# Optimization experiments

Hardware: AMD Instinct MI355X
Metric: run time of the kernel (lower is better)

Reference implementation:

```python
import jax, jax.numpy as jnp
import numpy as np

NUM_CLASSES = 19
TEMPERATURE = 0.2


def setup_inputs() -> dict:
    key = jax.random.key(0)
    k1, k2, k3 = jax.random.split(key, 3)
    fea = jax.random.normal(k1, (8, 256, 128, 128), dtype=jnp.float32)
    res = jax.random.normal(k2, (8, 19, 128, 128), dtype=jnp.float32)
    q = jax.random.normal(k3, (NUM_CLASSES, 256, 2975), dtype=jnp.float32)
    # buffers are L2-normalized along the feature (inner_planes) dim at init
    queues = q / jnp.maximum(jnp.linalg.norm(q, axis=1, keepdims=True), 1e-12)
    return {"fea": fea, "res": res, "queues": queues}


def _contrast_loss(fea, res, queues):
    # fea: [bs, C, H, W], res: [bs, K, H, W] logits, queues: [K, C, Q]
    bs, C = fea.shape[0], fea.shape[1]
    pred = jnp.argmax(res, axis=1).reshape(bs, -1)          # [bs, HW]
    ff = fea.reshape(bs, C, -1)                              # [bs, C, HW]

    # masked per-class region pooling across the whole batch (pred == val)
    onehot = (pred[:, :, None] == jnp.arange(NUM_CLASSES)[None, None, :]).astype(fea.dtype)  # [bs, HW, K]
    counts = onehot.sum(axis=(0, 1))                         # [K]
    sums = jnp.einsum('bcp,bpk->kc', ff, onehot)             # [K, C]
    keys = sums / jnp.maximum(counts, 1.0)[:, None]          # masked mean per class
    # F.normalize(keys, dim=1) with eps=1e-12
    keys = keys / jnp.maximum(jnp.linalg.norm(keys, axis=1, keepdims=True), 1e-12)

    # l_pos = q[:,None] * queue_c ; l_neg = q[:,None] * sum_{c'!=c} queue_c'
    qsum = queues.sum(axis=0)                                # [C, Q]
    l_pos = keys[:, :, None] * queues                        # [K, C, Q]
    l_neg = keys[:, :, None] * (qsum[None] - queues)         # [K, C, Q]
    logits = jnp.concatenate([l_pos, l_neg], axis=2) / TEMPERATURE  # [K, C, 2Q]

    # CrossEntropyLoss with labels all zero: mean over rows of (logsumexp - logit_0)
    lse = jax.nn.logsumexp(logits, axis=2)                   # [K, C]
    per_class = jnp.mean(lse - logits[:, :, 0], axis=1)      # [K]

    # original sums loss only over classes present in pred
    present = counts > 0
    return jnp.sum(jnp.where(present, per_class, jnp.zeros_like(per_class)))


def reference(fea, res, queues):
    contrast_loss = _contrast_loss(fea, res, queues)
    return (res, contrast_loss)
```

## Files before the change

kernel.cpp:

```cpp
#include <hip/hip_runtime.h>

#define HW 16384
#define BS 8
#define NC 256
#define K  19
#define Q  2975
#define INV_T 5.0f
#define NCHUNK 4
#define QC 744
#define NB1 512

__global__ void __launch_bounds__(256) k1_argmax(const float* __restrict__ res,
                                                 float* __restrict__ out,
                                                 unsigned char* __restrict__ pred,
                                                 int* __restrict__ histb,
                                                 float* __restrict__ sums) {
    __shared__ int hist[K];
    int t = threadIdx.x;
    if (t < K) hist[t] = 0;
    __syncthreads();
    int gp = blockIdx.x * 256 + t;
    int b  = gp >> 14;
    int p  = gp & (HW - 1);
    const float* rb = res + (size_t)b * K * HW + p;
    float*       ob = out + (size_t)b * K * HW + p;
    float best = rb[0];
    int   bk   = 0;
    ob[0] = best;
    #pragma unroll
    for (int k = 1; k < K; ++k) {
        float v = rb[(size_t)k * HW];
        ob[(size_t)k * HW] = v;
        if (v > best) { best = v; bk = k; }
    }
    pred[gp] = (unsigned char)bk;
    atomicAdd(&hist[bk], 1);
    if (blockIdx.x == 0) {
        for (int i = t; i < K * NC; i += 256) sums[i] = 0.f;
    }
    __syncthreads();
    if (t < K) histb[t * NB1 + blockIdx.x] = hist[t];
}

__global__ void __launch_bounds__(256) k2_pool(const float* __restrict__ fea,
                                               const unsigned char* __restrict__ pred,
                                               float* __restrict__ sums) {
    __shared__ float acc[K * 256];
    int t = threadIdx.x;
    int b = blockIdx.x >> 8;
    int c = blockIdx.x & 255;
    #pragma unroll
    for (int k = 0; k < K; ++k) acc[k * 256 + t] = 0.f;
    __syncthreads();
    const float4* f4 = (const float4*)(fea + (size_t)(b * NC + c) * HW);
    const uchar4* p4 = (const uchar4*)(pred + (size_t)b * HW);
    for (int i = t; i < HW / 4; i += 256) {
        float4 v  = f4[i];
        uchar4 kk = p4[i];
        acc[kk.x * 256 + t] += v.x;
        acc[kk.y * 256 + t] += v.y;
        acc[kk.z * 256 + t] += v.z;
        acc[kk.w * 256 + t] += v.w;
    }
    __syncthreads();
    for (int s = 128; s > 0; s >>= 1) {
        for (int idx = t; idx < K * s; idx += 256) {
            int k = idx / s, j = idx - k * s;
            acc[k * 256 + j] += acc[k * 256 + j + s];
        }
        __syncthreads();
    }
    if (t < K) atomicAdd(&sums[t * 256 + c], acc[t * 256]);
}

__global__ void k3_keys(const float* __restrict__ sums, const int* __restrict__ histb,
                        float* __restrict__ keys_t, float* __restrict__ countsf) {
    int t = threadIdx.x, lane = t & 63, w = t >> 6;
    const float4* s4 = (const float4*)sums;
    float4*       o4 = (float4*)keys_t;
    for (int k = w; k < K; k += 4) {
        float cf = 0.f;
        #pragma unroll
        for (int j = 0; j < NB1 / 64; ++j)
            cf += (float)histb[k * NB1 + j * 64 + lane];
        float4 v = s4[k * 64 + lane];
        float ss = v.x * v.x + v.y * v.y + v.z * v.z + v.w * v.w;
        #pragma unroll
        for (int off = 32; off > 0; off >>= 1) {
            ss += __shfl_xor(ss, off, 64);
            cf += __shfl_xor(cf, off, 64);
        }
        float denom = fmaxf(sqrtf(ss), fmaxf(cf, 1.0f) * 1e-12f);
        float sc = INV_T / denom;
        v.x *= sc; v.y *= sc; v.z *= sc; v.w *= sc;
        o4[k * 64 + lane] = v;
        if (lane == 0) countsf[k] = cf;
    }
}

__global__ void __launch_bounds__(256, 4) k4_lse(const float* __restrict__ queues,
                                                 const float* __restrict__ keys_t,
                                                 float* __restrict__ spart,
                                                 float* __restrict__ pos0) {
    int t = threadIdx.x;
    int c = blockIdx.x;
    int chunk = blockIdx.y;
    int lane = t & 63, wv = t >> 6;

    float key[K], s[K];
    #pragma unroll
    for (int k = 0; k < K; ++k) {
        key[k] = keys_t[k * NC + c];
        s[k] = 0.f;
    }
    if (chunk == 0 && t < K)
        pos0[t * NC + c] = keys_t[t * NC + c] * queues[(size_t)(t * NC + c) * Q];

    int q0 = chunk * QC;
    int qhi = min(Q, q0 + QC);
    for (int q = q0 + t; q < qhi; q += 256) {
        float qv[K];
        float qs = 0.f;
        #pragma unroll
        for (int k = 0; k < K; ++k) {
            qv[k] = queues[(size_t)(k * NC + c) * Q + q];
            qs += qv[k];
        }
        #pragma unroll
        for (int k = 0; k < K; ++k) {
            float a  = key[k] * qv[k];
            float bn = fmaf(key[k], qs, -a);
            s[k] += __expf(a) + __expf(bn);
        }
    }

    __shared__ float sw[K][4];
    #pragma unroll
    for (int k = 0; k < K; ++k) {
        float sk = s[k];
        #pragma unroll
        for (int off = 32; off > 0; off >>= 1) sk += __shfl_xor(sk, off, 64);
        if (lane == 0) sw[k][wv] = sk;
    }
    __syncthreads();
    if (t < K)
        spart[((size_t)t * NC + c) * NCHUNK + chunk] = sw[t][0] + sw[t][1] + sw[t][2] + sw[t][3];
}

__global__ void k5_final(const float* __restrict__ spart, const float* __restrict__ pos0,
                         const float* __restrict__ countsf, float* __restrict__ loss) {
    int t = threadIdx.x;
    float acc = 0.f;
    #pragma unroll
    for (int k = 0; k < K; ++k) {
        float4 sp = ((const float4*)spart)[k * NC + t];
        float lse = logf(sp.x + sp.y + sp.z + sp.w);
        if (countsf[k] > 0.5f) acc += lse - pos0[k * NC + t];
    }
    __shared__ float red[256];
    red[t] = acc;
    __syncthreads();
    for (int s = 128; s > 0; s >>= 1) {
        if (t < s) red[t] += red[t + s];
        __syncthreads();
    }
    if (t == 0) *loss = red[0] * (1.0f / 256.0f);
}

extern "C" void kernel_launch(void* const* d_in, const int* in_sizes, int n_in,
                              void* d_out, int out_size, void* d_ws, size_t ws_size,
                              hipStream_t stream) {
    const float* fea    = (const float*)d_in[0];
    const float* res    = (const float*)d_in[1];
    const float* queues = (const float*)d_in[2];

    float* out  = (float*)d_out;
    float* loss = out + (size_t)BS * K * HW;

    char* ws = (char*)d_ws;
    float*         sums   = (float*)(ws);
    int*           histb  = (int*)(ws + 19456);
    float*         countsf= (float*)(ws + 58368);
    unsigned char* pred   = (unsigned char*)(ws + 58496);
    float*         keys_t = (float*)(ws + 189568);
    float*         spart  = (float*)(ws + 209024);
    float*         pos0   = (float*)(ws + 286848);

    hipLaunchKernelGGL(k1_argmax, dim3(NB1),        dim3(256), 0, stream, res, out, pred, histb, sums);
    hipLaunchKernelGGL(k2_pool,   dim3(BS * NC),    dim3(256), 0, stream, fea, pred, sums);
    hipLaunchKernelGGL(k3_keys,   dim3(1),          dim3(256), 0, stream, sums, histb, keys_t, countsf);
    hipLaunchKernelGGL(k4_lse,    dim3(NC, NCHUNK), dim3(256), 0, stream, queues, keys_t, spart, pos0);
    hipLaunchKernelGGL(k5_final,  dim3(1),          dim3(256), 0, stream, spart, pos0, countsf, loss);
}
```

Before: 62.15 us.

## Fold key normalization into lse kernel and simplify pooling reduction

Removes the single-block keys kernel by having each lse block recompute per-class norms from the pooled sums into shared memory, and moves class-count summation into the final kernel. The pooling kernel's multi-step shared-memory tree reduction is replaced by a strided add plus wave shuffle with per-wave atomics. This drops a kernel launch and many block barriers, at the cost of redundant norm computation in every lse block.

```diff
diff --git a/kernel.cpp b/kernel.cpp
--- a/kernel.cpp
+++ b/kernel.cpp
@@ -46,7 +46,7 @@
                                                const unsigned char* __restrict__ pred,
                                                float* __restrict__ sums) {
     __shared__ float acc[K * 256];
-    int t = threadIdx.x;
+    int t = threadIdx.x, lane = t & 63, w = t >> 6;
     int b = blockIdx.x >> 8;
     int c = blockIdx.x & 255;
     #pragma unroll
@@ -63,43 +63,17 @@
         acc[kk.w * 256 + t] += v.w;
     }
     __syncthreads();
-    for (int s = 128; s > 0; s >>= 1) {
-        for (int idx = t; idx < K * s; idx += 256) {
-            int k = idx / s, j = idx - k * s;
-            acc[k * 256 + j] += acc[k * 256 + j + s];
-        }
-        __syncthreads();
-    }
-    if (t < K) atomicAdd(&sums[t * 256 + c], acc[t * 256]);
-}
-
-__global__ void k3_keys(const float* __restrict__ sums, const int* __restrict__ histb,
-                        float* __restrict__ keys_t, float* __restrict__ countsf) {
-    int t = threadIdx.x, lane = t & 63, w = t >> 6;
-    const float4* s4 = (const float4*)sums;
-    float4*       o4 = (float4*)keys_t;
     for (int k = w; k < K; k += 4) {
-        float cf = 0.f;
+        float v = acc[k * 256 + lane]       + acc[k * 256 + lane + 64]
+                + acc[k * 256 + lane + 128] + acc[k * 256 + lane + 192];
         #pragma unroll
-        for (int j = 0; j < NB1 / 64; ++j)
-            cf += (float)histb[k * NB1 + j * 64 + lane];
-        float4 v = s4[k * 64 + lane];
-        float ss = v.x * v.x + v.y * v.y + v.z * v.z + v.w * v.w;
-        #pragma unroll
-        for (int off = 32; off > 0; off >>= 1) {
-            ss += __shfl_xor(ss, off, 64);
-            cf += __shfl_xor(cf, off, 64);
-        }
-        float denom = fmaxf(sqrtf(ss), fmaxf(cf, 1.0f) * 1e-12f);
-        float sc = INV_T / denom;
-        v.x *= sc; v.y *= sc; v.z *= sc; v.w *= sc;
-        o4[k * 64 + lane] = v;
-        if (lane == 0) countsf[k] = cf;
+        for (int off = 32; off > 0; off >>= 1) v += __shfl_xor(v, off, 64);
+        if (lane == 0) atomicAdd(&sums[k * NC + c], v);
     }
 }
 
 __global__ void __launch_bounds__(256, 4) k4_lse(const float* __restrict__ queues,
-                                                 const float* __restrict__ keys_t,
+                                                 const float* __restrict__ sums,
                                                  float* __restrict__ spart,
                                                  float* __restrict__ pos0) {
     int t = threadIdx.x;
@@ -107,14 +81,28 @@
     int chunk = blockIdx.y;
     int lane = t & 63, wv = t >> 6;
 
+    __shared__ float sc_sh[K];
+    for (int k = wv; k < K; k += 4) {
+        float ss = 0.f;
+        #pragma unroll
+        for (int j = 0; j < 4; ++j) {
+            float v = sums[k * NC + j * 64 + lane];
+            ss += v * v;
+        }
+        #pragma unroll
+        for (int off = 32; off > 0; off >>= 1) ss += __shfl_xor(ss, off, 64);
+        if (lane == 0) sc_sh[k] = INV_T / fmaxf(sqrtf(ss), 1e-12f);
+    }
+    __syncthreads();
+
     float key[K], s[K];
     #pragma unroll
     for (int k = 0; k < K; ++k) {
-        key[k] = keys_t[k * NC + c];
+        key[k] = sums[k * NC + c] * sc_sh[k];
         s[k] = 0.f;
     }
     if (chunk == 0 && t < K)
-        pos0[t * NC + c] = keys_t[t * NC + c] * queues[(size_t)(t * NC + c) * Q];
+        pos0[t * NC + c] = sums[t * NC + c] * sc_sh[t] * queues[(size_t)(t * NC + c) * Q];
 
     int q0 = chunk * QC;
     int qhi = min(Q, q0 + QC);
@@ -148,14 +136,25 @@
 }
 
 __global__ void k5_final(const float* __restrict__ spart, const float* __restrict__ pos0,
-                         const float* __restrict__ countsf, float* __restrict__ loss) {
-    int t = threadIdx.x;
+                         const int* __restrict__ histb, float* __restrict__ loss) {
+    __shared__ float cnt_sh[K];
+    int t = threadIdx.x, lane = t & 63, w = t >> 6;
+    for (int k = w; k < K; k += 4) {
+        float cf = 0.f;
+        #pragma unroll
+        for (int j = 0; j < NB1 / 64; ++j)
+            cf += (float)histb[k * NB1 + j * 64 + lane];
+        #pragma unroll
+        for (int off = 32; off > 0; off >>= 1) cf += __shfl_xor(cf, off, 64);
+        if (lane == 0) cnt_sh[k] = cf;
+    }
+    __syncthreads();
     float acc = 0.f;
     #pragma unroll
     for (int k = 0; k < K; ++k) {
         float4 sp = ((const float4*)spart)[k * NC + t];
         float lse = logf(sp.x + sp.y + sp.z + sp.w);
-        if (countsf[k] > 0.5f) acc += lse - pos0[k * NC + t];
+        if (cnt_sh[k] > 0.5f) acc += lse - pos0[k * NC + t];
     }
     __shared__ float red[256];
     red[t] = acc;
@@ -180,15 +179,12 @@
     char* ws = (char*)d_ws;
     float*         sums   = (float*)(ws);
     int*           histb  = (int*)(ws + 19456);
-    float*         countsf= (float*)(ws + 58368);
-    unsigned char* pred   = (unsigned char*)(ws + 58496);
-    float*         keys_t = (float*)(ws + 189568);
-    float*         spart  = (float*)(ws + 209024);
-    float*         pos0   = (float*)(ws + 286848);
+    unsigned char* pred   = (unsigned char*)(ws + 58368);
+    float*         spart  = (float*)(ws + 189440);
+    float*         pos0   = (float*)(ws + 267264);
 
     hipLaunchKernelGGL(k1_argmax, dim3(NB1),        dim3(256), 0, stream, res, out, pred, histb, sums);
     hipLaunchKernelGGL(k2_pool,   dim3(BS * NC),    dim3(256), 0, stream, fea, pred, sums);
-    hipLaunchKernelGGL(k3_keys,   dim3(1),          dim3(256), 0, stream, sums, histb, keys_t, countsf);
-    hipLaunchKernelGGL(k4_lse,    dim3(NC, NCHUNK), dim3(256), 0, stream, queues, keys_t, spart, pos0);
-    hipLaunchKernelGGL(k5_final,  dim3(1),          dim3(256), 0, stream, spart, pos0, countsf, loss);
+    hipLaunchKernelGGL(k4_lse,    dim3(NC, NCHUNK), dim3(256), 0, stream, queues, sums, spart, pos0);
+    hipLaunchKernelGGL(k5_final,  dim3(1),          dim3(256), 0, stream, spart, pos0, histb, loss);
 }
```

After: 63.18 us. About the same (+1.7%).
